# Performance work log

Hardware: AMD Instinct MI355X
Metric: run time of the kernel (lower is better)

## Reference

```python
import jax, jax.numpy as jnp
import numpy as np
from jax import lax

THR = 1.0
BETA = 0.9
SLOPE = 25.0  # fast_sigmoid surrogate slope
N_JOINTS = 6

@jax.custom_vjp
def spike_fn(x):
    # Heaviside forward, fast_sigmoid surrogate backward (snntorch surrogate.fast_sigmoid)
    return (x > 0).astype(x.dtype)

def _spike_fwd(x):
    return spike_fn(x), x

def _spike_bwd(x, g):
    return (g / (SLOPE * jnp.abs(x) + 1.0) ** 2,)

spike_fn.defvjp(_spike_fwd, _spike_bwd)

def lif(cur, mem):
    # snntorch Leaky, reset_mechanism='subtract': reset from previous mem (detached)
    reset = lax.stop_gradient(spike_fn(mem - THR))
    mem = BETA * mem + cur - reset * THR
    spk = spike_fn(mem - THR)
    return spk, mem

def rate_encode(data, u):
    # data: (B, F), u: (T, B, F) uniform[0,1) -> binary spikes (T, B, F)
    dmin = jnp.min(data, axis=1, keepdims=True)
    dmax = jnp.max(data, axis=1, keepdims=True)
    rng = dmax - dmin
    rng = jnp.where(rng == 0, jnp.ones_like(rng), rng)
    norm = (data - dmin) / rng
    prob = jnp.clip(100.0 * norm * 0.001, 0.0, 1.0)  # max_rate=100, dt=0.001
    return (u < prob[None]).astype(jnp.float32)

def conv1x1(x, W, b):
    # x: (B, Cin, H, 1), W: (Cout, Cin, 1, 1)
    y = lax.conv_general_dilated(x, W, (1, 1), 'VALID',
                                 dimension_numbers=('NCHW', 'OIHW', 'NCHW'))
    return y + b[None, :, None, None]

def setup_inputs() -> dict:
    key = jax.random.key(0)
    ks = jax.random.split(key, 16)
    B, T, n = 8192, 200, N_JOINTS
    inp = {
        'x':  jax.random.normal(ks[0], (B, 3 * n), jnp.float32),
        'u1': jax.random.uniform(ks[1], (T, B, 2 * n), jnp.float32),
        'u2': jax.random.uniform(ks[2], (T, B, n), jnp.float32),
        'u3': jax.random.uniform(ks[3], (T, B, n), jnp.float32),
        'W1': jax.random.normal(ks[4], (256, 12), jnp.float32) * 0.2,
        'b1': jax.random.normal(ks[5], (256,), jnp.float32) * 0.05,
        'W2': jax.random.normal(ks[6], (256, 256), jnp.float32) * 0.06,
        'b2': jax.random.normal(ks[7], (256,), jnp.float32) * 0.05,
        'W3': jax.random.normal(ks[8], (6, 256), jnp.float32) * 0.06,
        'b3': jax.random.normal(ks[9], (6,), jnp.float32) * 0.05,
        'Wc1': jax.random.normal(ks[10], (32, 3, 1, 1), jnp.float32) * 0.5,
        'bc1': jax.random.normal(ks[11], (32,), jnp.float32) * 0.05,
        'Wc2': jax.random.normal(ks[12], (64, 32, 1, 1), jnp.float32) * 0.15,
        'bc2': jax.random.normal(ks[13], (64,), jnp.float32) * 0.05,
        'WA': jax.random.normal(ks[14], (1, 64), jnp.float32) * 0.12,
    }
    return inp

def reference(x, u1, u2, u3, W1, b1, W2, b2, W3, b3, Wc1, bc1, Wc2, bc2, WA):
    n = N_JOINTS
    B = x.shape[0]
    spk_in = rate_encode(x[:, :2 * n], u1)        # (T, B, 2n)
    spk_thdot = rate_encode(x[:, n:2 * n], u2)    # (T, B, n)
    spk_thdot2 = rate_encode(x[:, 2 * n:], u3)    # (T, B, n)

    mem1 = jnp.zeros((B, 256), jnp.float32)
    mem2 = jnp.zeros((B, 256), jnp.float32)
    mem3 = jnp.zeros((B, n), jnp.float32)
    mem4 = jnp.zeros((B, 32, n, 1), jnp.float32)
    conv_out0 = jnp.zeros((B, 64, n, 1), jnp.float32)

    def step(carry, inp):
        m1, m2, m3, m4, _ = carry
        s_in, s_td, s_td2 = inp
        spk1, m1 = lif(s_in @ W1.T + b1, m1)
        spk2, m2 = lif(spk1 @ W2.T + b2, m2)
        spk3, m3 = lif(spk2 @ W3.T + b3, m3)
        spk_conv = jnp.stack([s_td, spk3, s_td2], axis=1)[..., None]  # (B,3,n,1)
        cur4 = conv1x1(spk_conv, Wc1, bc1)  # maxpool1 with k=1 is identity
        spk4, m4 = lif(cur4, m4)
        conv_out = conv1x1(spk4, Wc2, bc2)  # maxpool2 with k=1 is identity
        return (m1, m2, m3, m4, conv_out), None

    (_, _, _, _, conv_out), _ = lax.scan(step, (mem1, mem2, mem3, mem4, conv_out0),
                                         (spk_in, spk_thdot, spk_thdot2))
    # c.T: out_a/b/c = fc_A(conv_out[:, :, i, 0]) for i in 0..2, no bias
    c_t = jnp.einsum('bcm,c->bm', conv_out[:, :, :3, 0], WA[0])  # (B, 3)
    return c_t
```

## Files before the change

kernel.cpp:

```cpp
#include <hip/hip_runtime.h>
#include <cstdint>
#include <cstddef>

typedef unsigned long long u64;

__global__ void prep_weights(const float* __restrict__ W1, const float* __restrict__ W2,
                             const float* __restrict__ W3, const float* __restrict__ Wc2,
                             const float* __restrict__ bc2, const float* __restrict__ WA,
                             float* __restrict__ Wt1, float* __restrict__ Wt2,
                             float* __restrict__ Wt3, double* __restrict__ wEff,
                             double* __restrict__ bEff)
{
  int id = blockIdx.x * 256 + (int)threadIdx.x;
  if (id < 65536){ int i = id >> 8, j = id & 255; Wt2[(i<<8)+j] = W2[j*256+i]; }
  if (id < 3072){ int k = id >> 8, j = id & 255; Wt1[(k<<8)+j] = W1[j*12+k]; }
  if (id < 1024){ int i = id >> 2, jj = id & 3; Wt3[id] = (jj<3) ? W3[jj*256+i] : 0.0f; }
  if (id < 32){ double s = 0.0; for (int c=0;c<64;c++) s += (double)WA[c]*(double)Wc2[c*32+id]; wEff[id] = s; }
  if (id == 32){ double s = 0.0; for (int c=0;c<64;c++) s += (double)WA[c]*(double)bc2[c]; *bEff = s; }
}

__global__ void prep_probs(const float* __restrict__ x, double* __restrict__ probs, int B)
{
  int b = blockIdx.x, k = (int)threadIdx.x;
  if (b >= B || k >= 24) return;
  double* pb = probs + (size_t)b*24;
  if (k >= 18){ pb[k] = -1.0; return; }
  int fk, g0, gn;
  if (k < 12){ fk = k;          g0 = 0;  gn = 12; }
  else if (k < 15){ fk = 6+(k-12);  g0 = 6;  gn = 6; }
  else           { fk = 12+(k-15); g0 = 12; gn = 6; }
  const float* xb = x + (size_t)b*18;
  double mn = (double)xb[g0], mx = mn;
  for (int f = 1; f < gn; f++){ double v = (double)xb[g0+f]; mn = fmin(mn, v); mx = fmax(mx, v); }
  double rng = mx - mn; if (rng == 0.0) rng = 1.0;
  double norm = ((double)xb[fk] - mn) / rng;
  double p = (100.0 * norm) * 0.001;
  p = fmin(fmax(p, 0.0), 1.0);
  pb[k] = p;
}

__global__ void prep_enc(const float* __restrict__ u1, const float* __restrict__ u2,
                         const float* __restrict__ u3, const double* __restrict__ probs,
                         unsigned* __restrict__ enc, int B)
{
  int b = blockIdx.x * blockDim.x + (int)threadIdx.x;
  int t = blockIdx.y;
  if (b >= B) return;
  const double* pb = probs + (size_t)b*24;
  size_t r = (size_t)t * B + b;
  const float* a1 = u1 + r*12;
  const float* a2 = u2 + r*6;
  const float* a3 = u3 + r*6;
  unsigned e = 0;
  #pragma unroll
  for (int k = 0; k < 12; k++) if ((double)a1[k] < pb[k])    e |= (1u << k);
  #pragma unroll
  for (int h = 0; h < 3; h++)  if ((double)a2[h] < pb[12+h]) e |= (1u << (12+h));
  #pragma unroll
  for (int h = 0; h < 3; h++)  if ((double)a3[h] < pb[15+h]) e |= (1u << (15+h));
  enc[r] = e;
}

__global__ __launch_bounds__(256) void snn_main(
    const unsigned* __restrict__ enc,
    const float* __restrict__ b1, const float* __restrict__ b2, const float* __restrict__ b3,
    const float* __restrict__ Wc1, const float* __restrict__ bc1,
    const float* __restrict__ Wt1, const float* __restrict__ Wt2, const float* __restrict__ Wt3,
    const double* __restrict__ wEff, const double* __restrict__ bEff,
    float* __restrict__ out, int B, int T)
{
  const int lane = (int)(threadIdx.x & 63);
  const int b = blockIdx.x * 4 + (int)(threadIdx.x >> 6);
  if (b >= B) return;
  const int l4 = lane << 2;

  const float4 b1f = *(const float4*)(b1 + l4);
  const float4 b2f = *(const float4*)(b2 + l4);
  const double b1d0=b1f.x, b1d1=b1f.y, b1d2=b1f.z, b1d3=b1f.w;
  const double b2d0=b2f.x, b2d1=b2f.y, b2d2=b2f.z, b2d3=b2f.w;
  const double b3d = (lane < 3) ? (double)b3[lane] : 0.0;
  double wc1a=0.0, wc1b=0.0, wc1c=0.0, bc1d=0.0, wEd=0.0;
  if (lane < 32){
    wc1a = (double)Wc1[lane*3+0];
    wc1b = (double)Wc1[lane*3+1];
    wc1c = (double)Wc1[lane*3+2];
    bc1d = (double)bc1[lane];
    wEd  = wEff[lane];
  }
  const float* __restrict__ w1base = Wt1 + l4;
  const float* __restrict__ w2base = Wt2 + l4;

  double m10=0,m11=0,m12=0,m13=0;
  double m20=0,m21=0,m22=0,m23=0;
  double m3v=0;
  double m40=0,m41=0,m42=0;

  for (int t = 0; t < T; t++){
    const unsigned e = enc[(size_t)t * B + b];
    const unsigned sm  = e & 0xFFFu;
    const unsigned td  = (e >> 12) & 7u;
    const unsigned td2 = (e >> 15) & 7u;

    double c0=b1d0, c1=b1d1, c2=b1d2, c3=b1d3;
    {
      unsigned w = sm;
      while (w){
        int k0 = __builtin_ctz(w); w &= w-1;
        int k1=k0,k2=k0,k3=k0,n=1;
        if (w){ k1=__builtin_ctz(w); w&=w-1; n=2;
          if (w){ k2=__builtin_ctz(w); w&=w-1; n=3;
            if (w){ k3=__builtin_ctz(w); w&=w-1; n=4; } } }
        const float4 r0 = *(const float4*)(w1base + (k0<<8));
        const float4 r1 = *(const float4*)(w1base + (k1<<8));
        const float4 r2 = *(const float4*)(w1base + (k2<<8));
        const float4 r3 = *(const float4*)(w1base + (k3<<8));
        c0 += (double)r0.x; c1 += (double)r0.y; c2 += (double)r0.z; c3 += (double)r0.w;
        if (n>1){ c0+=(double)r1.x; c1+=(double)r1.y; c2+=(double)r1.z; c3+=(double)r1.w; }
        if (n>2){ c0+=(double)r2.x; c1+=(double)r2.y; c2+=(double)r2.z; c3+=(double)r2.w; }
        if (n>3){ c0+=(double)r3.x; c1+=(double)r3.y; c2+=(double)r3.z; c3+=(double)r3.w; }
      }
    }
    bool rr;
    rr = m10>1.0; m10 = 0.9*m10 + c0; if (rr) m10 -= 1.0;
    rr = m11>1.0; m11 = 0.9*m11 + c1; if (rr) m11 -= 1.0;
    rr = m12>1.0; m12 = 0.9*m12 + c2; if (rr) m12 -= 1.0;
    rr = m13>1.0; m13 = 0.9*m13 + c3; if (rr) m13 -= 1.0;
    const u64 s1w0 = __ballot(m10 > 1.0);
    const u64 s1w1 = __ballot(m11 > 1.0);
    const u64 s1w2 = __ballot(m12 > 1.0);
    const u64 s1w3 = __ballot(m13 > 1.0);

    c0=b2d0; c1=b2d1; c2=b2d2; c3=b2d3;
#define L2LOOP(WREG, CW) { u64 w = (WREG); \
      while (w){ \
        int i0 = ((int)__builtin_ctzll(w)<<2)+(CW); w &= w-1; \
        int i1=i0,i2=i0,i3=i0,n=1; \
        if (w){ i1=((int)__builtin_ctzll(w)<<2)+(CW); w&=w-1; n=2; \
          if (w){ i2=((int)__builtin_ctzll(w)<<2)+(CW); w&=w-1; n=3; \
            if (w){ i3=((int)__builtin_ctzll(w)<<2)+(CW); w&=w-1; n=4; } } } \
        const float4 r0 = *(const float4*)(w2base + (i0<<8)); \
        const float4 r1 = *(const float4*)(w2base + (i1<<8)); \
        const float4 r2 = *(const float4*)(w2base + (i2<<8)); \
        const float4 r3 = *(const float4*)(w2base + (i3<<8)); \
        c0 += (double)r0.x; c1 += (double)r0.y; c2 += (double)r0.z; c3 += (double)r0.w; \
        if (n>1){ c0+=(double)r1.x; c1+=(double)r1.y; c2+=(double)r1.z; c3+=(double)r1.w; } \
        if (n>2){ c0+=(double)r2.x; c1+=(double)r2.y; c2+=(double)r2.z; c3+=(double)r2.w; } \
        if (n>3){ c0+=(double)r3.x; c1+=(double)r3.y; c2+=(double)r3.z; c3+=(double)r3.w; } \
      } }
    L2LOOP(s1w0, 0)
    L2LOOP(s1w1, 1)
    L2LOOP(s1w2, 2)
    L2LOOP(s1w3, 3)

    rr = m20>1.0; m20 = 0.9*m20 + c0; if (rr) m20 -= 1.0;
    rr = m21>1.0; m21 = 0.9*m21 + c1; if (rr) m21 -= 1.0;
    rr = m22>1.0; m22 = 0.9*m22 + c2; if (rr) m22 -= 1.0;
    rr = m23>1.0; m23 = 0.9*m23 + c3; if (rr) m23 -= 1.0;
    const u64 s2w0 = __ballot(m20 > 1.0);
    const u64 s2w1 = __ballot(m21 > 1.0);
    const u64 s2w2 = __ballot(m22 > 1.0);
    const u64 s2w3 = __ballot(m23 > 1.0);

    double cl3 = b3d;
#define L3LOOP(WREG, CW) { u64 w = (WREG); \
      while (w){ \
        int i0 = ((int)__builtin_ctzll(w)<<2)+(CW); w &= w-1; \
        int i1=i0,i2=i0,i3=i0,n=1; \
        if (w){ i1=((int)__builtin_ctzll(w)<<2)+(CW); w&=w-1; n=2; \
          if (w){ i2=((int)__builtin_ctzll(w)<<2)+(CW); w&=w-1; n=3; \
            if (w){ i3=((int)__builtin_ctzll(w)<<2)+(CW); w&=w-1; n=4; } } } \
        float q0=0.f,q1=0.f,q2=0.f,q3=0.f; \
        if (lane < 3){ q0 = Wt3[(i0<<2)+lane]; q1 = Wt3[(i1<<2)+lane]; \
                       q2 = Wt3[(i2<<2)+lane]; q3 = Wt3[(i3<<2)+lane]; } \
        cl3 += (double)q0; \
        if (n>1) cl3 += (double)q1; \
        if (n>2) cl3 += (double)q2; \
        if (n>3) cl3 += (double)q3; \
      } }
    L3LOOP(s2w0, 0)
    L3LOOP(s2w1, 1)
    L3LOOP(s2w2, 2)
    L3LOOP(s2w3, 3)

    rr = m3v>1.0; m3v = 0.9*m3v + cl3; if (rr) m3v -= 1.0;
    const unsigned s3 = (unsigned)(__ballot((lane < 3) && (m3v > 1.0)) & 7ull);

    double cur;
    cur = bc1d; if (td  & 1u) cur += wc1a; if (s3 & 1u) cur += wc1b; if (td2 & 1u) cur += wc1c;
    rr = m40>1.0; m40 = 0.9*m40 + cur; if (rr) m40 -= 1.0;
    cur = bc1d; if (td  & 2u) cur += wc1a; if (s3 & 2u) cur += wc1b; if (td2 & 2u) cur += wc1c;
    rr = m41>1.0; m41 = 0.9*m41 + cur; if (rr) m41 -= 1.0;
    cur = bc1d; if (td  & 4u) cur += wc1a; if (s3 & 4u) cur += wc1b; if (td2 & 4u) cur += wc1c;
    rr = m42>1.0; m42 = 0.9*m42 + cur; if (rr) m42 -= 1.0;
  }

  double o0 = (lane < 32 && m40 > 1.0) ? wEd : 0.0;
  double o1 = (lane < 32 && m41 > 1.0) ? wEd : 0.0;
  double o2 = (lane < 32 && m42 > 1.0) ? wEd : 0.0;
  for (int off = 32; off > 0; off >>= 1){
    o0 += __shfl_xor(o0, off, 64);
    o1 += __shfl_xor(o1, off, 64);
    o2 += __shfl_xor(o2, off, 64);
  }
  if (lane == 0){
    const double be = *bEff;
    out[b*3+0] = (float)(o0 + be);
    out[b*3+1] = (float)(o1 + be);
    out[b*3+2] = (float)(o2 + be);
  }
}

extern "C" void kernel_launch(void* const* d_in, const int* in_sizes, int n_in,
                              void* d_out, int out_size, void* d_ws, size_t ws_size,
                              hipStream_t stream)
{
  const float* x   = (const float*)d_in[0];
  const float* u1  = (const float*)d_in[1];
  const float* u2  = (const float*)d_in[2];
  const float* u3  = (const float*)d_in[3];
  const float* W1  = (const float*)d_in[4];
  const float* b1  = (const float*)d_in[5];
  const float* W2  = (const float*)d_in[6];
  const float* b2  = (const float*)d_in[7];
  const float* W3  = (const float*)d_in[8];
  const float* b3  = (const float*)d_in[9];
  const float* Wc1 = (const float*)d_in[10];
  const float* bc1 = (const float*)d_in[11];
  const float* Wc2 = (const float*)d_in[12];
  const float* bc2 = (const float*)d_in[13];
  const float* WA  = (const float*)d_in[14];
  float* out = (float*)d_out;

  const int B = in_sizes[0] / 18;
  const int T = in_sizes[1] / (B * 12);

  char* ws = (char*)d_ws;
  float*  Wt2   = (float*)(ws + 0);
  float*  Wt1   = (float*)(ws + 262144);
  float*  Wt3   = (float*)(ws + 274432);
  double* wEff  = (double*)(ws + 278528);
  double* bEff  = (double*)(ws + 278784);
  double* probs = (double*)(ws + 278792);
  unsigned* enc = (unsigned*)(ws + 278792 + (size_t)B*24*8);

  hipLaunchKernelGGL(prep_weights, dim3(256), dim3(256), 0, stream,
                     W1, W2, W3, Wc2, bc2, WA, Wt1, Wt2, Wt3, wEff, bEff);
  hipLaunchKernelGGL(prep_probs, dim3(B), dim3(64), 0, stream, x, probs, B);
  hipLaunchKernelGGL(prep_enc, dim3((B+255)/256, T), dim3(256), 0, stream,
                     u1, u2, u3, probs, enc, B);
  hipLaunchKernelGGL(snn_main, dim3((B+3)/4), dim3(256), 0, stream,
                     enc, b1, b2, b3, Wc1, bc1, Wt1, Wt2, Wt3, wEff, bEff, out, B, T);
}
```

Before: 850.1 us.

## Store transposed weights as doubles and prefetch next encoded spike word

Pre-transposed weight tables are now stored as fp64, so the inner accumulation loops load double2 pairs directly instead of converting floats to doubles on every gathered row. The next timestep's encoded spike word is prefetched during the current step and made wave-uniform with readfirstlane. The LIF resets are turned into branchless precomputed reset flags, and the layer-1 gather is narrowed to two rows per iteration. The cost is twice the weight bytes (512KB for W2), which puts more pressure on cache bandwidth.

```diff
diff --git a/kernel.cpp b/kernel.cpp
--- a/kernel.cpp
+++ b/kernel.cpp
@@ -7,14 +7,14 @@
 __global__ void prep_weights(const float* __restrict__ W1, const float* __restrict__ W2,
                              const float* __restrict__ W3, const float* __restrict__ Wc2,
                              const float* __restrict__ bc2, const float* __restrict__ WA,
-                             float* __restrict__ Wt1, float* __restrict__ Wt2,
-                             float* __restrict__ Wt3, double* __restrict__ wEff,
+                             double* __restrict__ Wt1, double* __restrict__ Wt2,
+                             double* __restrict__ Wt3, double* __restrict__ wEff,
                              double* __restrict__ bEff)
 {
   int id = blockIdx.x * 256 + (int)threadIdx.x;
-  if (id < 65536){ int i = id >> 8, j = id & 255; Wt2[(i<<8)+j] = W2[j*256+i]; }
-  if (id < 3072){ int k = id >> 8, j = id & 255; Wt1[(k<<8)+j] = W1[j*12+k]; }
-  if (id < 1024){ int i = id >> 2, jj = id & 3; Wt3[id] = (jj<3) ? W3[jj*256+i] : 0.0f; }
+  if (id < 65536){ int i = id >> 8, j = id & 255; Wt2[(i<<8)+j] = (double)W2[j*256+i]; }
+  if (id < 3072){ int k = id >> 8, j = id & 255; Wt1[(k<<8)+j] = (double)W1[j*12+k]; }
+  if (id < 1024){ int i = id >> 2, jj = id & 3; Wt3[id] = (jj<3) ? (double)W3[jj*256+i] : 0.0; }
   if (id < 32){ double s = 0.0; for (int c=0;c<64;c++) s += (double)WA[c]*(double)Wc2[c*32+id]; wEff[id] = s; }
   if (id == 32){ double s = 0.0; for (int c=0;c<64;c++) s += (double)WA[c]*(double)bc2[c]; *bEff = s; }
 }
@@ -65,7 +65,7 @@
     const unsigned* __restrict__ enc,
     const float* __restrict__ b1, const float* __restrict__ b2, const float* __restrict__ b3,
     const float* __restrict__ Wc1, const float* __restrict__ bc1,
-    const float* __restrict__ Wt1, const float* __restrict__ Wt2, const float* __restrict__ Wt3,
+    const double* __restrict__ Wt1, const double* __restrict__ Wt2, const double* __restrict__ Wt3,
     const double* __restrict__ wEff, const double* __restrict__ bEff,
     float* __restrict__ out, int B, int T)
 {
@@ -73,6 +73,7 @@
   const int b = blockIdx.x * 4 + (int)(threadIdx.x >> 6);
   if (b >= B) return;
   const int l4 = lane << 2;
+  const int lcl = (lane < 3) ? lane : 3;
 
   const float4 b1f = *(const float4*)(b1 + l4);
   const float4 b2f = *(const float4*)(b2 + l4);
@@ -87,16 +88,21 @@
     bc1d = (double)bc1[lane];
     wEd  = wEff[lane];
   }
-  const float* __restrict__ w1base = Wt1 + l4;
-  const float* __restrict__ w2base = Wt2 + l4;
 
   double m10=0,m11=0,m12=0,m13=0;
   double m20=0,m21=0,m22=0,m23=0;
   double m3v=0;
   double m40=0,m41=0,m42=0;
+  double r10=0,r11=0,r12=0,r13=0;
+  double r20=0,r21=0,r22=0,r23=0;
+  double r3v=0;
+  double r40=0,r41=0,r42=0;
+
+  const unsigned* ep = enc + b;
+  unsigned e = __builtin_amdgcn_readfirstlane(*ep);
 
   for (int t = 0; t < T; t++){
-    const unsigned e = enc[(size_t)t * B + b];
+    unsigned e_nx = (t+1 < T) ? ep[(size_t)(t+1) * B] : 0u;
     const unsigned sm  = e & 0xFFFu;
     const unsigned td  = (e >> 12) & 7u;
     const unsigned td2 = (e >> 15) & 7u;
@@ -106,97 +112,105 @@
       unsigned w = sm;
       while (w){
         int k0 = __builtin_ctz(w); w &= w-1;
-        int k1=k0,k2=k0,k3=k0,n=1;
-        if (w){ k1=__builtin_ctz(w); w&=w-1; n=2;
-          if (w){ k2=__builtin_ctz(w); w&=w-1; n=3;
-            if (w){ k3=__builtin_ctz(w); w&=w-1; n=4; } } }
-        const float4 r0 = *(const float4*)(w1base + (k0<<8));
-        const float4 r1 = *(const float4*)(w1base + (k1<<8));
-        const float4 r2 = *(const float4*)(w1base + (k2<<8));
-        const float4 r3 = *(const float4*)(w1base + (k3<<8));
-        c0 += (double)r0.x; c1 += (double)r0.y; c2 += (double)r0.z; c3 += (double)r0.w;
-        if (n>1){ c0+=(double)r1.x; c1+=(double)r1.y; c2+=(double)r1.z; c3+=(double)r1.w; }
-        if (n>2){ c0+=(double)r2.x; c1+=(double)r2.y; c2+=(double)r2.z; c3+=(double)r2.w; }
-        if (n>3){ c0+=(double)r3.x; c1+=(double)r3.y; c2+=(double)r3.z; c3+=(double)r3.w; }
+        int k1 = k0; int n = 1;
+        if (w){ k1 = __builtin_ctz(w); w &= w-1; n = 2; }
+        const double* rp0 = Wt1 + ((size_t)k0 << 8);
+        const double* rp1 = Wt1 + ((size_t)k1 << 8);
+        double2 a0 = *(const double2*)(rp0 + l4);
+        double2 a1 = *(const double2*)(rp0 + l4 + 2);
+        double2 a2 = *(const double2*)(rp1 + l4);
+        double2 a3 = *(const double2*)(rp1 + l4 + 2);
+        c0 += a0.x; c1 += a0.y; c2 += a1.x; c3 += a1.y;
+        if (n > 1){ c0 += a2.x; c1 += a2.y; c2 += a3.x; c3 += a3.y; }
       }
     }
-    bool rr;
-    rr = m10>1.0; m10 = 0.9*m10 + c0; if (rr) m10 -= 1.0;
-    rr = m11>1.0; m11 = 0.9*m11 + c1; if (rr) m11 -= 1.0;
-    rr = m12>1.0; m12 = 0.9*m12 + c2; if (rr) m12 -= 1.0;
-    rr = m13>1.0; m13 = 0.9*m13 + c3; if (rr) m13 -= 1.0;
-    const u64 s1w0 = __ballot(m10 > 1.0);
-    const u64 s1w1 = __ballot(m11 > 1.0);
-    const u64 s1w2 = __ballot(m12 > 1.0);
-    const u64 s1w3 = __ballot(m13 > 1.0);
+    m10 = 0.9*m10 + c0; m10 -= r10;
+    m11 = 0.9*m11 + c1; m11 -= r11;
+    m12 = 0.9*m12 + c2; m12 -= r12;
+    m13 = 0.9*m13 + c3; m13 -= r13;
+    bool sp;
+    sp = m10 > 1.0; const u64 s1w0 = __ballot(sp); r10 = sp ? 1.0 : 0.0;
+    sp = m11 > 1.0; const u64 s1w1 = __ballot(sp); r11 = sp ? 1.0 : 0.0;
+    sp = m12 > 1.0; const u64 s1w2 = __ballot(sp); r12 = sp ? 1.0 : 0.0;
+    sp = m13 > 1.0; const u64 s1w3 = __ballot(sp); r13 = sp ? 1.0 : 0.0;
 
     c0=b2d0; c1=b2d1; c2=b2d2; c3=b2d3;
 #define L2LOOP(WREG, CW) { u64 w = (WREG); \
       while (w){ \
         int i0 = ((int)__builtin_ctzll(w)<<2)+(CW); w &= w-1; \
-        int i1=i0,i2=i0,i3=i0,n=1; \
+        int i1=i0,i2=i0,i3=i0; int n=1; \
         if (w){ i1=((int)__builtin_ctzll(w)<<2)+(CW); w&=w-1; n=2; \
           if (w){ i2=((int)__builtin_ctzll(w)<<2)+(CW); w&=w-1; n=3; \
             if (w){ i3=((int)__builtin_ctzll(w)<<2)+(CW); w&=w-1; n=4; } } } \
-        const float4 r0 = *(const float4*)(w2base + (i0<<8)); \
-        const float4 r1 = *(const float4*)(w2base + (i1<<8)); \
-        const float4 r2 = *(const float4*)(w2base + (i2<<8)); \
-        const float4 r3 = *(const float4*)(w2base + (i3<<8)); \
-        c0 += (double)r0.x; c1 += (double)r0.y; c2 += (double)r0.z; c3 += (double)r0.w; \
-        if (n>1){ c0+=(double)r1.x; c1+=(double)r1.y; c2+=(double)r1.z; c3+=(double)r1.w; } \
-        if (n>2){ c0+=(double)r2.x; c1+=(double)r2.y; c2+=(double)r2.z; c3+=(double)r2.w; } \
-        if (n>3){ c0+=(double)r3.x; c1+=(double)r3.y; c2+=(double)r3.z; c3+=(double)r3.w; } \
+        const double* rp0 = Wt2 + ((size_t)i0 << 8); \
+        const double* rp1 = Wt2 + ((size_t)i1 << 8); \
+        const double* rp2 = Wt2 + ((size_t)i2 << 8); \
+        const double* rp3 = Wt2 + ((size_t)i3 << 8); \
+        double2 aa0 = *(const double2*)(rp0 + l4), ab0 = *(const double2*)(rp0 + l4 + 2); \
+        double2 aa1 = *(const double2*)(rp1 + l4), ab1 = *(const double2*)(rp1 + l4 + 2); \
+        double2 aa2 = *(const double2*)(rp2 + l4), ab2 = *(const double2*)(rp2 + l4 + 2); \
+        double2 aa3 = *(const double2*)(rp3 + l4), ab3 = *(const double2*)(rp3 + l4 + 2); \
+        c0 += aa0.x; c1 += aa0.y; c2 += ab0.x; c3 += ab0.y; \
+        if (n>1){ c0 += aa1.x; c1 += aa1.y; c2 += ab1.x; c3 += ab1.y; } \
+        if (n>2){ c0 += aa2.x; c1 += aa2.y; c2 += ab2.x; c3 += ab2.y; } \
+        if (n>3){ c0 += aa3.x; c1 += aa3.y; c2 += ab3.x; c3 += ab3.y; } \
       } }
     L2LOOP(s1w0, 0)
     L2LOOP(s1w1, 1)
     L2LOOP(s1w2, 2)
     L2LOOP(s1w3, 3)
 
-    rr = m20>1.0; m20 = 0.9*m20 + c0; if (rr) m20 -= 1.0;
-    rr = m21>1.0; m21 = 0.9*m21 + c1; if (rr) m21 -= 1.0;
-    rr = m22>1.0; m22 = 0.9*m22 + c2; if (rr) m22 -= 1.0;
-    rr = m23>1.0; m23 = 0.9*m23 + c3; if (rr) m23 -= 1.0;
-    const u64 s2w0 = __ballot(m20 > 1.0);
-    const u64 s2w1 = __ballot(m21 > 1.0);
-    const u64 s2w2 = __ballot(m22 > 1.0);
-    const u64 s2w3 = __ballot(m23 > 1.0);
+    m20 = 0.9*m20 + c0; m20 -= r20;
+    m21 = 0.9*m21 + c1; m21 -= r21;
+    m22 = 0.9*m22 + c2; m22 -= r22;
+    m23 = 0.9*m23 + c3; m23 -= r23;
+    sp = m20 > 1.0; const u64 s2w0 = __ballot(sp); r20 = sp ? 1.0 : 0.0;
+    sp = m21 > 1.0; const u64 s2w1 = __ballot(sp); r21 = sp ? 1.0 : 0.0;
+    sp = m22 > 1.0; const u64 s2w2 = __ballot(sp); r22 = sp ? 1.0 : 0.0;
+    sp = m23 > 1.0; const u64 s2w3 = __ballot(sp); r23 = sp ? 1.0 : 0.0;
 
     double cl3 = b3d;
 #define L3LOOP(WREG, CW) { u64 w = (WREG); \
       while (w){ \
         int i0 = ((int)__builtin_ctzll(w)<<2)+(CW); w &= w-1; \
-        int i1=i0,i2=i0,i3=i0,n=1; \
+        int i1=i0,i2=i0,i3=i0; int n=1; \
         if (w){ i1=((int)__builtin_ctzll(w)<<2)+(CW); w&=w-1; n=2; \
           if (w){ i2=((int)__builtin_ctzll(w)<<2)+(CW); w&=w-1; n=3; \
             if (w){ i3=((int)__builtin_ctzll(w)<<2)+(CW); w&=w-1; n=4; } } } \
-        float q0=0.f,q1=0.f,q2=0.f,q3=0.f; \
-        if (lane < 3){ q0 = Wt3[(i0<<2)+lane]; q1 = Wt3[(i1<<2)+lane]; \
-                       q2 = Wt3[(i2<<2)+lane]; q3 = Wt3[(i3<<2)+lane]; } \
-        cl3 += (double)q0; \
-        if (n>1) cl3 += (double)q1; \
-        if (n>2) cl3 += (double)q2; \
-        if (n>3) cl3 += (double)q3; \
+        const double* q0 = Wt3 + ((size_t)i0 << 2); \
+        const double* q1 = Wt3 + ((size_t)i1 << 2); \
+        const double* q2 = Wt3 + ((size_t)i2 << 2); \
+        const double* q3 = Wt3 + ((size_t)i3 << 2); \
+        double v0 = q0[lcl], v1 = q1[lcl], v2 = q2[lcl], v3 = q3[lcl]; \
+        cl3 += v0; \
+        if (n>1) cl3 += v1; \
+        if (n>2) cl3 += v2; \
+        if (n>3) cl3 += v3; \
       } }
     L3LOOP(s2w0, 0)
     L3LOOP(s2w1, 1)
     L3LOOP(s2w2, 2)
     L3LOOP(s2w3, 3)
 
-    rr = m3v>1.0; m3v = 0.9*m3v + cl3; if (rr) m3v -= 1.0;
-    const unsigned s3 = (unsigned)(__ballot((lane < 3) && (m3v > 1.0)) & 7ull);
+    m3v = 0.9*m3v + cl3; m3v -= r3v;
+    sp = m3v > 1.0;
+    const unsigned s3 = (unsigned)(__ballot((lane < 3) && sp) & 7ull);
+    r3v = sp ? 1.0 : 0.0;
 
     double cur;
-    cur = bc1d; if (td  & 1u) cur += wc1a; if (s3 & 1u) cur += wc1b; if (td2 & 1u) cur += wc1c;
-    rr = m40>1.0; m40 = 0.9*m40 + cur; if (rr) m40 -= 1.0;
-    cur = bc1d; if (td  & 2u) cur += wc1a; if (s3 & 2u) cur += wc1b; if (td2 & 2u) cur += wc1c;
-    rr = m41>1.0; m41 = 0.9*m41 + cur; if (rr) m41 -= 1.0;
-    cur = bc1d; if (td  & 4u) cur += wc1a; if (s3 & 4u) cur += wc1b; if (td2 & 4u) cur += wc1c;
-    rr = m42>1.0; m42 = 0.9*m42 + cur; if (rr) m42 -= 1.0;
-  }
-
-  double o0 = (lane < 32 && m40 > 1.0) ? wEd : 0.0;
-  double o1 = (lane < 32 && m41 > 1.0) ? wEd : 0.0;
-  double o2 = (lane < 32 && m42 > 1.0) ? wEd : 0.0;
+    cur = bc1d + ((td  & 1u) ? wc1a : 0.0) + ((s3 & 1u) ? wc1b : 0.0) + ((td2 & 1u) ? wc1c : 0.0);
+    m40 = 0.9*m40 + cur; m40 -= r40; r40 = (m40 > 1.0) ? 1.0 : 0.0;
+    cur = bc1d + ((td  & 2u) ? wc1a : 0.0) + ((s3 & 2u) ? wc1b : 0.0) + ((td2 & 2u) ? wc1c : 0.0);
+    m41 = 0.9*m41 + cur; m41 -= r41; r41 = (m41 > 1.0) ? 1.0 : 0.0;
+    cur = bc1d + ((td  & 4u) ? wc1a : 0.0) + ((s3 & 4u) ? wc1b : 0.0) + ((td2 & 4u) ? wc1c : 0.0);
+    m42 = 0.9*m42 + cur; m42 -= r42; r42 = (m42 > 1.0) ? 1.0 : 0.0;
+
+    e = __builtin_amdgcn_readfirstlane(e_nx);
+  }
+
+  double o0 = r40 * wEd;
+  double o1 = r41 * wEd;
+  double o2 = r42 * wEd;
   for (int off = 32; off > 0; off >>= 1){
     o0 += __shfl_xor(o0, off, 64);
     o1 += __shfl_xor(o1, off, 64);
@@ -235,13 +249,13 @@
   const int T = in_sizes[1] / (B * 12);
 
   char* ws = (char*)d_ws;
-  float*  Wt2   = (float*)(ws + 0);
-  float*  Wt1   = (float*)(ws + 262144);
-  float*  Wt3   = (float*)(ws + 274432);
-  double* wEff  = (double*)(ws + 278528);
-  double* bEff  = (double*)(ws + 278784);
-  double* probs = (double*)(ws + 278792);
-  unsigned* enc = (unsigned*)(ws + 278792 + (size_t)B*24*8);
+  double* Wt2   = (double*)(ws + 0);
+  double* Wt1   = (double*)(ws + 524288);
+  double* Wt3   = (double*)(ws + 548864);
+  double* wEff  = (double*)(ws + 557056);
+  double* bEff  = (double*)(ws + 557312);
+  double* probs = (double*)(ws + 557320);
+  unsigned* enc = (unsigned*)(ws + 557320 + (size_t)B*24*8);
 
   hipLaunchKernelGGL(prep_weights, dim3(256), dim3(256), 0, stream,
                      W1, W2, W3, Wc2, bc2, WA, Wt1, Wt2, Wt3, wEff, bEff);
```

Result: slower. 876.6 us (+3.1%).
